# Performance work log

Measured on AMD Instinct MI355X. Metric: run time of the kernel, lower is better.

## Reference

```python
import jax, jax.numpy as jnp
import numpy as np

N = 100000      # nodes
E = 1600000     # edges
IN = 128        # in_channels
HID = 64        # hidden_channels
HEADS = 2       # gat_heads
NEG_SLOPE = 0.2 # PyG GATConv default leaky_relu slope


def setup_inputs() -> dict:
    key = jax.random.key(0)
    ks = jax.random.split(key, 8)
    x = jax.random.normal(ks[0], (N, IN), jnp.float32)
    edge_index = jax.random.randint(ks[1], (2, E), 0, N, jnp.int32)
    edge_weight = jax.random.uniform(ks[2], (E,), jnp.float32)
    gcn_w = jax.random.normal(ks[3], (IN, HID), jnp.float32) * (1.0 / np.sqrt(IN))
    gcn_b = jnp.zeros((HID,), jnp.float32)
    gat_w = jax.random.normal(ks[4], (HID, HEADS * HID), jnp.float32) * (1.0 / np.sqrt(HID))
    att_src = jax.random.normal(ks[5], (HEADS, HID), jnp.float32) * 0.1
    att_dst = jax.random.normal(ks[6], (HEADS, HID), jnp.float32) * 0.1
    gat_b = jnp.zeros((HID,), jnp.float32)
    return {"x": x, "edge_index": edge_index, "edge_weight": edge_weight,
            "gcn_w": gcn_w, "gcn_b": gcn_b, "gat_w": gat_w,
            "att_src": att_src, "att_dst": att_dst, "gat_b": gat_b}


def _gcn(x, w, b, src, dst, ew, n):
    # PyG GCNConv: add self-loops (weight 1), symmetric deg^{-1/2} norm.
    loop = jnp.arange(n, dtype=src.dtype)
    s = jnp.concatenate([src, loop])
    d = jnp.concatenate([dst, loop])
    wt = jnp.concatenate([ew, jnp.ones((n,), ew.dtype)])
    deg = jax.ops.segment_sum(wt, d, num_segments=n)              # in-degree (weighted)
    dinv = jnp.where(deg > 0, jax.lax.rsqrt(jnp.maximum(deg, 1e-12)), 0.0)
    norm = dinv[s] * wt * dinv[d]                                  # [E+N]
    h = x @ w                                                      # [N, HID]
    out = jax.ops.segment_sum(norm[:, None] * h[s], d, num_segments=n)
    return out + b


def _gat(x, w, a_src, a_dst, b, src, dst, n):
    # PyG GATConv: additive attention, self-loops, segment softmax over dst.
    h = (x @ w).reshape(n, HEADS, HID)                             # [N,H,C]
    score_s = jnp.einsum('nhc,hc->nh', h, a_src)                   # [N,H]
    score_d = jnp.einsum('nhc,hc->nh', h, a_dst)                   # [N,H]
    loop = jnp.arange(n, dtype=src.dtype)
    s = jnp.concatenate([src, loop])
    d = jnp.concatenate([dst, loop])
    alpha = score_s[s] + score_d[d]                                # [E+N,H]
    alpha = jnp.where(alpha >= 0, alpha, NEG_SLOPE * alpha)        # leaky_relu
    amax = jax.lax.stop_gradient(jax.ops.segment_max(alpha, d, num_segments=n))
    ex = jnp.exp(alpha - amax[d])
    denom = jax.ops.segment_sum(ex, d, num_segments=n)
    coef = ex / jnp.maximum(denom[d], 1e-16)                       # [E+N,H]
    out = jax.ops.segment_sum(coef[:, :, None] * h[s], d, num_segments=n)  # [N,H,C]
    return out.mean(axis=1) + b                                    # concat=False -> mean


def reference(x, edge_index, edge_weight, gcn_w, gcn_b, gat_w, att_src, att_dst, gat_b):
    src, dst = edge_index[0], edge_index[1]
    n = x.shape[0]
    h = jax.nn.relu(_gcn(x, gcn_w, gcn_b, src, dst, edge_weight, n))
    out = jax.nn.relu(_gat(h, gat_w, att_src, att_dst, gat_b, src, dst, n))
    return out
```

## Files before the change

kernel.cpp:

```cpp
#include <hip/hip_runtime.h>
#include <hip/hip_fp16.h>
#include <math.h>

#define N_NODES 100000
#define N_EDGES 1600000
#define IN_CH 128
#define HID 64
#define HEADS 2
#define NEG_SLOPE 0.2f

#define NB_SCAN ((N_NODES + 255) / 256)
#define SHARD_SZ 12500

static __device__ inline ushort f2h(float f) { return __half_as_ushort(__float2half(f)); }
static __device__ inline float h2f(ushort u) { return __half2float(__ushort_as_half(u)); }
static __device__ inline void h8f(uint4 u, float f[8]) {
    f[0] = h2f((ushort)(u.x & 0xffff)); f[1] = h2f((ushort)(u.x >> 16));
    f[2] = h2f((ushort)(u.y & 0xffff)); f[3] = h2f((ushort)(u.y >> 16));
    f[4] = h2f((ushort)(u.z & 0xffff)); f[5] = h2f((ushort)(u.z >> 16));
    f[6] = h2f((ushort)(u.w & 0xffff)); f[7] = h2f((ushort)(u.w >> 16));
}
static __device__ inline uint pack2(float a, float b) {
    return (uint)f2h(a) | ((uint)f2h(b) << 16);
}

__device__ inline float leaky(float a) { return (a >= 0.0f) ? a : NEG_SLOPE * a; }


__global__ void k_count(const int* __restrict__ dst, int* count) {
    int e = blockIdx.x * 256 + threadIdx.x;
    if (e < N_EDGES) atomicAdd(&count[dst[e]], 1);
}

__global__ void k_scan_a(const int* __restrict__ count, int* __restrict__ incl,
                         int* __restrict__ bsum) {
    __shared__ int sh[256];
    int tid = threadIdx.x;
    int g = blockIdx.x * 256 + tid;
    int v = (g < N_NODES) ? count[g] : 0;
    sh[tid] = v;
    __syncthreads();
    for (int off = 1; off < 256; off <<= 1) {
        int t = (tid >= off) ? sh[tid - off] : 0;
        __syncthreads();
        sh[tid] += t;
        __syncthreads();
    }
    if (g < N_NODES) incl[g] = sh[tid];
    if (tid == 255) bsum[blockIdx.x] = sh[255];
}

__global__ void k_scan_b(const int* __restrict__ bsum, int* __restrict__ boff) {
    __shared__ int sh[512];
    int tid = threadIdx.x;
    int v = (tid < NB_SCAN) ? bsum[tid] : 0;
    sh[tid] = v;
    __syncthreads();
    for (int off = 1; off < 512; off <<= 1) {
        int t = (tid >= off) ? sh[tid - off] : 0;
        __syncthreads();
        sh[tid] += t;
        __syncthreads();
    }
    if (tid < NB_SCAN) boff[tid] = sh[tid] - v;
}

__global__ void k_scan_c(const int* __restrict__ count, const int* __restrict__ incl,
                         const int* __restrict__ boff, int* rowptr, int* cursor) {
    int g = blockIdx.x * 256 + threadIdx.x;
    if (g >= N_NODES) return;
    int excl = incl[g] - count[g] + boff[blockIdx.x];
    rowptr[g] = excl;
    cursor[g] = excl;
    if (g == N_NODES - 1) rowptr[N_NODES] = incl[g] + boff[blockIdx.x];
}

__global__ void k_scatter(const int* __restrict__ src, const int* __restrict__ dst,
                          const float* __restrict__ ew,
                          int* cursor, int2* __restrict__ ep) {
    int shard = blockIdx.x & 7;
    int e = (blockIdx.x >> 3) * 256 + threadIdx.x;
    if (e >= N_EDGES) return;
    int d = dst[e];
    if (d / SHARD_SZ != shard) return;
    int pos = atomicAdd(&cursor[d], 1);
    ep[pos] = make_int2(src[e], __float_as_int(ew[e]));
}

__global__ void k_deg_dinv(const int* __restrict__ rowptr, const int2* __restrict__ ep,
                           float* __restrict__ dinv) {
    int n = blockIdx.x * 256 + threadIdx.x;
    if (n >= N_NODES) return;
    int r0 = rowptr[n], r1 = rowptr[n + 1];
    float deg = 1.0f;
    for (int i = r0; i < r1; ++i) deg += __int_as_float(ep[i].y);
    dinv[n] = rsqrtf(deg);
}


__global__ __launch_bounds__(256) void k_gemm1(const float* __restrict__ x,
                                               const float* __restrict__ w,
                                               ushort4* __restrict__ h1h) {
    __shared__ float sxT[64][65];
    __shared__ float sw[128][64];
    int t = threadIdx.x;
    int tx = t & 15, ty = t >> 4;
    int row0 = blockIdx.x * 64;
    for (int i = t; i < 128 * 16; i += 256)
        ((float4*)sw)[i] = ((const float4*)w)[i];
    float acc[4][4] = {};
    for (int c = 0; c < 2; ++c) {
        __syncthreads();
        for (int i = t; i < 64 * 16; i += 256) {
            int r = i >> 4, kq = i & 15;
            int row = row0 + r;
            float4 v = make_float4(0.f, 0.f, 0.f, 0.f);
            if (row < N_NODES) v = ((const float4*)x)[row * 32 + c * 16 + kq];
            int k = kq * 4;
            sxT[k][r] = v.x; sxT[k + 1][r] = v.y; sxT[k + 2][r] = v.z; sxT[k + 3][r] = v.w;
        }
        __syncthreads();
        #pragma unroll 8
        for (int k = 0; k < 64; ++k) {
            float a0 = sxT[k][ty * 4], a1 = sxT[k][ty * 4 + 1];
            float a2 = sxT[k][ty * 4 + 2], a3 = sxT[k][ty * 4 + 3];
            float4 bb = *(const float4*)&sw[c * 64 + k][tx * 4];
            acc[0][0] += a0 * bb.x; acc[0][1] += a0 * bb.y; acc[0][2] += a0 * bb.z; acc[0][3] += a0 * bb.w;
            acc[1][0] += a1 * bb.x; acc[1][1] += a1 * bb.y; acc[1][2] += a1 * bb.z; acc[1][3] += a1 * bb.w;
            acc[2][0] += a2 * bb.x; acc[2][1] += a2 * bb.y; acc[2][2] += a2 * bb.z; acc[2][3] += a2 * bb.w;
            acc[3][0] += a3 * bb.x; acc[3][1] += a3 * bb.y; acc[3][2] += a3 * bb.z; acc[3][3] += a3 * bb.w;
        }
    }
    #pragma unroll
    for (int i = 0; i < 4; ++i) {
        int row = row0 + ty * 4 + i;
        if (row < N_NODES) {
            ushort4 o;
            o.x = f2h(acc[i][0]); o.y = f2h(acc[i][1]); o.z = f2h(acc[i][2]); o.w = f2h(acc[i][3]);
            h1h[row * 16 + tx] = o;
        }
    }
}

__global__ __launch_bounds__(256) void k_gemm2(const uint4* __restrict__ a16,
                                               const float* __restrict__ w,
                                               const float* __restrict__ att_src,
                                               const float* __restrict__ att_dst,
                                               ushort4* __restrict__ h2h,
                                               float* __restrict__ ss, float* __restrict__ sd) {
    __shared__ float sxT[64][65];
    __shared__ float swh[64][64];
    int t = threadIdx.x;
    int tx = t & 15, ty = t >> 4;
    int tile = blockIdx.x >> 1, half = blockIdx.x & 1;
    int row0 = tile * 64;
    for (int i = t; i < 64 * 16; i += 256) {
        int k = i >> 4, cq = i & 15;
        float4 v = ((const float4*)(w + k * 128 + half * 64))[cq];
        ((float4*)&swh[k][cq * 4])[0] = v;
    }
    for (int i = t; i < 64 * 8; i += 256) {
        int r = i >> 3, j = i & 7;
        int row = row0 + r;
        float f[8] = {};
        if (row < N_NODES) { uint4 u = a16[row * 8 + j]; h8f(u, f); }
        int k = j * 8;
        #pragma unroll
        for (int m = 0; m < 8; ++m) sxT[k + m][r] = f[m];
    }
    __syncthreads();
    float acc[4][4] = {};
    #pragma unroll 8
    for (int k = 0; k < 64; ++k) {
        float a0 = sxT[k][ty * 4], a1 = sxT[k][ty * 4 + 1];
        float a2 = sxT[k][ty * 4 + 2], a3 = sxT[k][ty * 4 + 3];
        float4 bb = *(const float4*)&swh[k][tx * 4];
        acc[0][0] += a0 * bb.x; acc[0][1] += a0 * bb.y; acc[0][2] += a0 * bb.z; acc[0][3] += a0 * bb.w;
        acc[1][0] += a1 * bb.x; acc[1][1] += a1 * bb.y; acc[1][2] += a1 * bb.z; acc[1][3] += a1 * bb.w;
        acc[2][0] += a2 * bb.x; acc[2][1] += a2 * bb.y; acc[2][2] += a2 * bb.z; acc[2][3] += a2 * bb.w;
        acc[3][0] += a3 * bb.x; acc[3][1] += a3 * bb.y; acc[3][2] += a3 * bb.z; acc[3][3] += a3 * bb.w;
    }
    float as0 = att_src[half * 64 + tx * 4],     as1 = att_src[half * 64 + tx * 4 + 1];
    float as2 = att_src[half * 64 + tx * 4 + 2], as3 = att_src[half * 64 + tx * 4 + 3];
    float ad0 = att_dst[half * 64 + tx * 4],     ad1 = att_dst[half * 64 + tx * 4 + 1];
    float ad2 = att_dst[half * 64 + tx * 4 + 2], ad3 = att_dst[half * 64 + tx * 4 + 3];
    #pragma unroll
    for (int i = 0; i < 4; ++i) {
        int row = row0 + ty * 4 + i;
        float ps = acc[i][0] * as0 + acc[i][1] * as1 + acc[i][2] * as2 + acc[i][3] * as3;
        float pd = acc[i][0] * ad0 + acc[i][1] * ad1 + acc[i][2] * ad2 + acc[i][3] * ad3;
        #pragma unroll
        for (int off = 1; off < 16; off <<= 1) {
            ps += __shfl_xor(ps, off, 64);
            pd += __shfl_xor(pd, off, 64);
        }
        if (row < N_NODES) {
            if (tx == 0) { ss[row * 2 + half] = ps; sd[row * 2 + half] = pd; }
            ushort4 o;
            o.x = f2h(acc[i][0]); o.y = f2h(acc[i][1]); o.z = f2h(acc[i][2]); o.w = f2h(acc[i][3]);
            h2h[row * 32 + half * 16 + tx] = o;
        }
    }
}


__global__ void k_gcn_csr(const int* __restrict__ rowptr, const int2* __restrict__ ep,
                          const float* __restrict__ dinv,
                          const uint4* __restrict__ h1q, const float* __restrict__ b,
                          uint4* __restrict__ agg1h) {
    int t = threadIdx.x;
    int n = blockIdx.x * 4 + (t >> 6);
    if (n >= N_NODES) return;
    int lane = t & 63, q = lane >> 3, r = lane & 7;
    int r0 = rowptr[n], r1 = rowptr[n + 1];
    float dn = dinv[n];
    float acc[8] = {};
    if (q == 0) {
        float f[8]; h8f(h1q[n * 8 + r], f);
        #pragma unroll
        for (int j = 0; j < 8; ++j) acc[j] = dn * f[j];
    }
    for (int i = r0 + q; i < r1; i += 8) {
        int2 e = ep[i];
        float wl = dinv[e.x] * __int_as_float(e.y);
        float f[8]; h8f(h1q[e.x * 8 + r], f);
        #pragma unroll
        for (int j = 0; j < 8; ++j) acc[j] += wl * f[j];
    }
    #pragma unroll
    for (int off = 8; off < 64; off <<= 1) {
        #pragma unroll
        for (int j = 0; j < 8; ++j) acc[j] += __shfl_xor(acc[j], off, 64);
    }
    if (q == 0) {
        float4 b0 = ((const float4*)b)[2 * r], b1 = ((const float4*)b)[2 * r + 1];
        float v0 = fmaxf(acc[0] * dn + b0.x, 0.f), v1 = fmaxf(acc[1] * dn + b0.y, 0.f);
        float v2 = fmaxf(acc[2] * dn + b0.z, 0.f), v3 = fmaxf(acc[3] * dn + b0.w, 0.f);
        float v4 = fmaxf(acc[4] * dn + b1.x, 0.f), v5 = fmaxf(acc[5] * dn + b1.y, 0.f);
        float v6 = fmaxf(acc[6] * dn + b1.z, 0.f), v7 = fmaxf(acc[7] * dn + b1.w, 0.f);
        uint4 o;
        o.x = pack2(v0, v1); o.y = pack2(v2, v3); o.z = pack2(v4, v5); o.w = pack2(v6, v7);
        agg1h[n * 8 + r] = o;
    }
}

__global__ void k_gat_csr(const int* __restrict__ rowptr, const int2* __restrict__ ep,
                          const float* __restrict__ ss, const float* __restrict__ sd,
                          const uint4* __restrict__ h2q, const float* __restrict__ b,
                          float* __restrict__ out) {
    int t = threadIdx.x;
    int n = blockIdx.x * 4 + (t >> 6);
    if (n >= N_NODES) return;
    int lane = t & 63;
    int g = lane >> 4;
    int t16 = lane & 15;
    int head = t16 >> 3;
    int r = t16 & 7;
    int r0 = rowptr[n], r1 = rowptr[n + 1];
    float sdn = sd[n * 2 + head];
    float den = 0.f;
    float acc[8] = {};
    if (g == 0) {
        float exs = __expf(leaky(ss[n * 2 + head] + sdn));
        den = exs;
        float f[8]; h8f(h2q[n * 16 + t16], f);
        #pragma unroll
        for (int j = 0; j < 8; ++j) acc[j] = exs * f[j];
    }
    for (int i = r0 + g; i < r1; i += 4) {
        int s = ep[i].x;
        float ex = __expf(leaky(ss[s * 2 + head] + sdn));
        den += ex;
        float f[8]; h8f(h2q[s * 16 + t16], f);
        #pragma unroll
        for (int j = 0; j < 8; ++j) acc[j] += ex * f[j];
    }
    #pragma unroll
    for (int off = 16; off < 64; off <<= 1) {
        #pragma unroll
        for (int j = 0; j < 8; ++j) acc[j] += __shfl_xor(acc[j], off, 64);
        den += __shfl_xor(den, off, 64);
    }
    float inv = 1.0f / fmaxf(den, 1e-16f);
    #pragma unroll
    for (int j = 0; j < 8; ++j) acc[j] *= inv;
    float o[8];
    #pragma unroll
    for (int j = 0; j < 8; ++j) o[j] = 0.5f * (acc[j] + __shfl_xor(acc[j], 8, 64));
    if (g == 0 && head == 0) {
        float4 b0 = ((const float4*)b)[2 * r], b1 = ((const float4*)b)[2 * r + 1];
        float4* op = (float4*)(out + n * 64 + r * 8);
        op[0] = make_float4(fmaxf(o[0] + b0.x, 0.f), fmaxf(o[1] + b0.y, 0.f),
                            fmaxf(o[2] + b0.z, 0.f), fmaxf(o[3] + b0.w, 0.f));
        op[1] = make_float4(fmaxf(o[4] + b1.x, 0.f), fmaxf(o[5] + b1.y, 0.f),
                            fmaxf(o[6] + b1.z, 0.f), fmaxf(o[7] + b1.w, 0.f));
    }
}

extern "C" void kernel_launch(void* const* d_in, const int* in_sizes, int n_in,
                              void* d_out, int out_size, void* d_ws, size_t ws_size,
                              hipStream_t stream) {
    const float* x       = (const float*)d_in[0];
    const int*   eidx    = (const int*)d_in[1];
    const float* ew      = (const float*)d_in[2];
    const float* gcn_w   = (const float*)d_in[3];
    const float* gcn_b   = (const float*)d_in[4];
    const float* gat_w   = (const float*)d_in[5];
    const float* att_src = (const float*)d_in[6];
    const float* att_dst = (const float*)d_in[7];
    const float* gat_b   = (const float*)d_in[8];
    float* out = (float*)d_out;

    const int* src = eidx;
    const int* dst = eidx + N_EDGES;

    char* p = (char*)d_ws;
    ushort* agg1h = (ushort*)p; p += sizeof(ushort) * (size_t)N_NODES * 64;
    ushort* h1h   = (ushort*)p; p += sizeof(ushort) * (size_t)N_NODES * 64;
    ushort* h2h   = (ushort*)p; p += sizeof(ushort) * (size_t)N_NODES * 128;
    int2*  ep     = (int2*)p;   p += sizeof(int2) * (size_t)N_EDGES;
    int*   count  = (int*)p;    p += sizeof(int) * N_NODES;
    float* dinv   = (float*)p;  p += sizeof(float) * N_NODES;
    int*   incl   = (int*)p;    p += sizeof(int) * N_NODES;
    int*   rowptr = (int*)p;    p += sizeof(int) * (N_NODES + 1);
    int*   cursor = (int*)p;    p += sizeof(int) * N_NODES;
    float* ss     = (float*)p;  p += sizeof(float) * N_NODES * 2;
    float* sd     = (float*)p;  p += sizeof(float) * N_NODES * 2;
    int*   bsum   = (int*)p;    p += sizeof(int) * NB_SCAN;
    int*   boff   = (int*)p;    p += sizeof(int) * NB_SCAN;

    const int T = 256;
    const int NBe  = (N_EDGES + T - 1) / T;
    const int NBe8 = 8 * NBe;

    hipMemsetAsync(count, 0, sizeof(int) * N_NODES, stream);
    k_count<<<NBe, T, 0, stream>>>(dst, count);
    k_scan_a<<<NB_SCAN, T, 0, stream>>>(count, incl, bsum);
    k_scan_b<<<1, 512, 0, stream>>>(bsum, boff);
    k_scan_c<<<NB_SCAN, T, 0, stream>>>(count, incl, boff, rowptr, cursor);
    k_scatter<<<NBe8, T, 0, stream>>>(src, dst, ew, cursor, ep);
    k_deg_dinv<<<NB_SCAN, T, 0, stream>>>(rowptr, ep, dinv);

    k_gemm1<<<(N_NODES + 63) / 64, T, 0, stream>>>(x, gcn_w, (ushort4*)h1h);
    k_gcn_csr<<<(N_NODES + 3) / 4, T, 0, stream>>>(rowptr, ep, dinv, (const uint4*)h1h, gcn_b, (uint4*)agg1h);

    k_gemm2<<<((N_NODES + 63) / 64) * 2, T, 0, stream>>>((const uint4*)agg1h, gat_w, att_src, att_dst, (ushort4*)h2h, ss, sd);
    k_gat_csr<<<(N_NODES + 3) / 4, T, 0, stream>>>(rowptr, ep, ss, sd, (const uint4*)h2h, gat_b, out);
}
```

Measured before the change: 444.1 us.

## Record per-edge rank during counting to build CSR without scatter atomics

The counting pass now saves each edge's atomic return value as a rank and accumulates weighted degree with a float atomic. The scatter pass then computes positions directly from rowptr plus rank, with no cursor atomics and no 8-way sharded grid that re-read every edge eight times. The separate degree kernel is removed, and dinv is computed in the scan finalisation. The cost is an extra rank array write and read plus a float atomic per edge, and the order of float degree accumulation becomes nondeterministic.

```diff
diff --git a/kernel.cpp b/kernel.cpp
--- a/kernel.cpp
+++ b/kernel.cpp
@@ -10,7 +10,6 @@
 #define NEG_SLOPE 0.2f
 
 #define NB_SCAN ((N_NODES + 255) / 256)
-#define SHARD_SZ 12500
 
 static __device__ inline ushort f2h(float f) { return __half_as_ushort(__float2half(f)); }
 static __device__ inline float h2f(ushort u) { return __half2float(__ushort_as_half(u)); }
@@ -27,9 +26,13 @@
 __device__ inline float leaky(float a) { return (a >= 0.0f) ? a : NEG_SLOPE * a; }
 
 
-__global__ void k_count(const int* __restrict__ dst, int* count) {
+__global__ void k_count(const int* __restrict__ dst, const float* __restrict__ ew,
+                        int* count, float* degf, ushort* __restrict__ rank) {
     int e = blockIdx.x * 256 + threadIdx.x;
-    if (e < N_EDGES) atomicAdd(&count[dst[e]], 1);
+    if (e >= N_EDGES) return;
+    int d = dst[e];
+    rank[e] = (ushort)atomicAdd(&count[d], 1);
+    atomicAdd(&degf[d], ew[e]);
 }
 
 __global__ void k_scan_a(const int* __restrict__ count, int* __restrict__ incl,
@@ -66,35 +69,24 @@
 }
 
 __global__ void k_scan_c(const int* __restrict__ count, const int* __restrict__ incl,
-                         const int* __restrict__ boff, int* rowptr, int* cursor) {
+                         const int* __restrict__ boff, const float* __restrict__ degf,
+                         int* rowptr, float* __restrict__ dinv) {
     int g = blockIdx.x * 256 + threadIdx.x;
     if (g >= N_NODES) return;
     int excl = incl[g] - count[g] + boff[blockIdx.x];
     rowptr[g] = excl;
-    cursor[g] = excl;
+    dinv[g] = rsqrtf(1.0f + degf[g]);
     if (g == N_NODES - 1) rowptr[N_NODES] = incl[g] + boff[blockIdx.x];
 }
 
 __global__ void k_scatter(const int* __restrict__ src, const int* __restrict__ dst,
-                          const float* __restrict__ ew,
-                          int* cursor, int2* __restrict__ ep) {
-    int shard = blockIdx.x & 7;
-    int e = (blockIdx.x >> 3) * 256 + threadIdx.x;
+                          const float* __restrict__ ew, const ushort* __restrict__ rank,
+                          const int* __restrict__ rowptr, int2* __restrict__ ep) {
+    int e = blockIdx.x * 256 + threadIdx.x;
     if (e >= N_EDGES) return;
     int d = dst[e];
-    if (d / SHARD_SZ != shard) return;
-    int pos = atomicAdd(&cursor[d], 1);
+    int pos = rowptr[d] + (int)rank[e];
     ep[pos] = make_int2(src[e], __float_as_int(ew[e]));
-}
-
-__global__ void k_deg_dinv(const int* __restrict__ rowptr, const int2* __restrict__ ep,
-                           float* __restrict__ dinv) {
-    int n = blockIdx.x * 256 + threadIdx.x;
-    if (n >= N_NODES) return;
-    int r0 = rowptr[n], r1 = rowptr[n + 1];
-    float deg = 1.0f;
-    for (int i = r0; i < r1; ++i) deg += __int_as_float(ep[i].y);
-    dinv[n] = rsqrtf(deg);
 }
 
 
@@ -320,26 +312,25 @@
     ushort* h2h   = (ushort*)p; p += sizeof(ushort) * (size_t)N_NODES * 128;
     int2*  ep     = (int2*)p;   p += sizeof(int2) * (size_t)N_EDGES;
     int*   count  = (int*)p;    p += sizeof(int) * N_NODES;
+    float* degf   = (float*)p;  p += sizeof(float) * N_NODES;
     float* dinv   = (float*)p;  p += sizeof(float) * N_NODES;
     int*   incl   = (int*)p;    p += sizeof(int) * N_NODES;
     int*   rowptr = (int*)p;    p += sizeof(int) * (N_NODES + 1);
-    int*   cursor = (int*)p;    p += sizeof(int) * N_NODES;
     float* ss     = (float*)p;  p += sizeof(float) * N_NODES * 2;
     float* sd     = (float*)p;  p += sizeof(float) * N_NODES * 2;
     int*   bsum   = (int*)p;    p += sizeof(int) * NB_SCAN;
     int*   boff   = (int*)p;    p += sizeof(int) * NB_SCAN;
+    ushort* rank  = (ushort*)p; p += sizeof(ushort) * (size_t)N_EDGES;
 
     const int T = 256;
-    const int NBe  = (N_EDGES + T - 1) / T;
-    const int NBe8 = 8 * NBe;
-
-    hipMemsetAsync(count, 0, sizeof(int) * N_NODES, stream);
-    k_count<<<NBe, T, 0, stream>>>(dst, count);
+    const int NBe = (N_EDGES + T - 1) / T;
+
+    hipMemsetAsync(count, 0, sizeof(int) * N_NODES + sizeof(float) * N_NODES, stream);
+    k_count<<<NBe, T, 0, stream>>>(dst, ew, count, degf, rank);
     k_scan_a<<<NB_SCAN, T, 0, stream>>>(count, incl, bsum);
     k_scan_b<<<1, 512, 0, stream>>>(bsum, boff);
-    k_scan_c<<<NB_SCAN, T, 0, stream>>>(count, incl, boff, rowptr, cursor);
-    k_scatter<<<NBe8, T, 0, stream>>>(src, dst, ew, cursor, ep);
-    k_deg_dinv<<<NB_SCAN, T, 0, stream>>>(rowptr, ep, dinv);
+    k_scan_c<<<NB_SCAN, T, 0, stream>>>(count, incl, boff, degf, rowptr, dinv);
+    k_scatter<<<NBe, T, 0, stream>>>(src, dst, ew, rank, rowptr, ep);
 
     k_gemm1<<<(N_NODES + 63) / 64, T, 0, stream>>>(x, gcn_w, (ushort4*)h1h);
     k_gcn_csr<<<(N_NODES + 3) / 4, T, 0, stream>>>(rowptr, ep, dinv, (const uint4*)h1h, gcn_b, (uint4*)agg1h);
```

New measurement: 487.1 us. +9.7%, slower.

## Replace atomic CSR build with chunked LDS histogram and deterministic rank scatter

Applied to the files above, without the earlier changes.

Builds the CSR with a chunked counting sort instead of global atomics. Each block histograms one edge chunk for one node shard in shared memory and records each edge's 8-bit rank and per-chunk counts. A per-node prefix over chunks plus the global scan then gives every edge a deterministic slot, so the scatter needs no atomic cursor and no memset. This adds extra byte-table traffic (NCHUNK x N bytes) and assumes per-chunk, per-node counts fit in 8 bits.

```diff
diff --git a/kernel.cpp b/kernel.cpp
--- a/kernel.cpp
+++ b/kernel.cpp
@@ -10,7 +10,10 @@
 #define NEG_SLOPE 0.2f
 
 #define NB_SCAN ((N_NODES + 255) / 256)
-#define SHARD_SZ 12500
+#define SHARD 12500
+#define CHUNK_E 32768
+#define NCHUNK ((N_EDGES + CHUNK_E - 1) / CHUNK_E)
+#define BLK_PER_CHUNK (CHUNK_E / 256)
 
 static __device__ inline ushort f2h(float f) { return __half_as_ushort(__float2half(f)); }
 static __device__ inline float h2f(ushort u) { return __half2float(__ushort_as_half(u)); }
@@ -26,18 +29,46 @@
 
 __device__ inline float leaky(float a) { return (a >= 0.0f) ? a : NEG_SLOPE * a; }
 
-
-__global__ void k_count(const int* __restrict__ dst, int* count) {
-    int e = blockIdx.x * 256 + threadIdx.x;
-    if (e < N_EDGES) atomicAdd(&count[dst[e]], 1);
-}
-
-__global__ void k_scan_a(const int* __restrict__ count, int* __restrict__ incl,
-                         int* __restrict__ bsum) {
+__global__ __launch_bounds__(256) void k_hist(const int* __restrict__ dst,
+                                              unsigned char* __restrict__ rank8,
+                                              unsigned char* __restrict__ ctab8) {
+    __shared__ uint bins[SHARD];
+    int c = blockIdx.x >> 3, s = blockIdx.x & 7;
+    int base = s * SHARD;
+    for (int i = threadIdx.x; i < SHARD; i += 256) bins[i] = 0;
+    __syncthreads();
+    int e0 = c * CHUNK_E;
+    int e1 = e0 + CHUNK_E; if (e1 > N_EDGES) e1 = N_EDGES;
+    for (int e = e0 + threadIdx.x; e < e1; e += 256) {
+        int local = dst[e] - base;
+        if ((unsigned)local < SHARD) {
+            uint old = atomicAdd(&bins[local], 1u);
+            rank8[e] = (unsigned char)old;
+        }
+    }
+    __syncthreads();
+    unsigned char* cc = ctab8 + (size_t)c * N_NODES + base;
+    for (int i = threadIdx.x; i < SHARD; i += 256) cc[i] = (unsigned char)bins[i];
+}
+
+__global__ void k_scan_a(unsigned char* __restrict__ ctab8,
+                         int* __restrict__ cntN,
+                         int* __restrict__ incl, int* __restrict__ bsum) {
     __shared__ int sh[256];
     int tid = threadIdx.x;
     int g = blockIdx.x * 256 + tid;
-    int v = (g < N_NODES) ? count[g] : 0;
+    int v = 0;
+    if (g < N_NODES) {
+        int run = 0;
+        size_t idx = (size_t)g;
+        for (int c = 0; c < NCHUNK; ++c, idx += N_NODES) {
+            int cnt = ctab8[idx];
+            ctab8[idx] = (unsigned char)run;
+            run += cnt;
+        }
+        v = run;
+        cntN[g] = run;
+    }
     sh[tid] = v;
     __syncthreads();
     for (int off = 1; off < 256; off <<= 1) {
@@ -65,25 +96,30 @@
     if (tid < NB_SCAN) boff[tid] = sh[tid] - v;
 }
 
-__global__ void k_scan_c(const int* __restrict__ count, const int* __restrict__ incl,
-                         const int* __restrict__ boff, int* rowptr, int* cursor) {
+__global__ void k_scan_c(const int* __restrict__ cntN, const int* __restrict__ incl,
+                         const int* __restrict__ boff, int* rowptr) {
     int g = blockIdx.x * 256 + threadIdx.x;
     if (g >= N_NODES) return;
-    int excl = incl[g] - count[g] + boff[blockIdx.x];
+    int excl = incl[g] - cntN[g] + boff[blockIdx.x];
     rowptr[g] = excl;
-    cursor[g] = excl;
     if (g == N_NODES - 1) rowptr[N_NODES] = incl[g] + boff[blockIdx.x];
 }
 
 __global__ void k_scatter(const int* __restrict__ src, const int* __restrict__ dst,
                           const float* __restrict__ ew,
-                          int* cursor, int2* __restrict__ ep) {
-    int shard = blockIdx.x & 7;
-    int e = (blockIdx.x >> 3) * 256 + threadIdx.x;
+                          const unsigned char* __restrict__ rank8,
+                          const unsigned char* __restrict__ ctab8,
+                          const int* __restrict__ rowptr, int2* __restrict__ ep) {
+    int b = blockIdx.x;
+    int x = b & 7;
+    int g = b >> 3;
+    int j = g & (BLK_PER_CHUNK - 1);
+    int c = (g >> 7) * 8 + x;
+    if (c >= NCHUNK) return;
+    int e = c * CHUNK_E + j * 256 + threadIdx.x;
     if (e >= N_EDGES) return;
     int d = dst[e];
-    if (d / SHARD_SZ != shard) return;
-    int pos = atomicAdd(&cursor[d], 1);
+    int pos = rowptr[d] + (int)ctab8[(size_t)c * N_NODES + d] + (int)rank8[e];
     ep[pos] = make_int2(src[e], __float_as_int(ew[e]));
 }
 
@@ -319,26 +355,24 @@
     ushort* h1h   = (ushort*)p; p += sizeof(ushort) * (size_t)N_NODES * 64;
     ushort* h2h   = (ushort*)p; p += sizeof(ushort) * (size_t)N_NODES * 128;
     int2*  ep     = (int2*)p;   p += sizeof(int2) * (size_t)N_EDGES;
-    int*   count  = (int*)p;    p += sizeof(int) * N_NODES;
     float* dinv   = (float*)p;  p += sizeof(float) * N_NODES;
     int*   incl   = (int*)p;    p += sizeof(int) * N_NODES;
+    int*   cntN   = (int*)p;    p += sizeof(int) * N_NODES;
     int*   rowptr = (int*)p;    p += sizeof(int) * (N_NODES + 1);
-    int*   cursor = (int*)p;    p += sizeof(int) * N_NODES;
     float* ss     = (float*)p;  p += sizeof(float) * N_NODES * 2;
     float* sd     = (float*)p;  p += sizeof(float) * N_NODES * 2;
     int*   bsum   = (int*)p;    p += sizeof(int) * NB_SCAN;
     int*   boff   = (int*)p;    p += sizeof(int) * NB_SCAN;
+    unsigned char* ctab8 = (unsigned char*)p; p += (size_t)NCHUNK * N_NODES;
+    unsigned char* rank8 = (unsigned char*)p; p += (size_t)N_EDGES;
 
     const int T = 256;
-    const int NBe  = (N_EDGES + T - 1) / T;
-    const int NBe8 = 8 * NBe;
-
-    hipMemsetAsync(count, 0, sizeof(int) * N_NODES, stream);
-    k_count<<<NBe, T, 0, stream>>>(dst, count);
-    k_scan_a<<<NB_SCAN, T, 0, stream>>>(count, incl, bsum);
+
+    k_hist<<<NCHUNK * 8, T, 0, stream>>>(dst, rank8, ctab8);
+    k_scan_a<<<NB_SCAN, T, 0, stream>>>(ctab8, cntN, incl, bsum);
     k_scan_b<<<1, 512, 0, stream>>>(bsum, boff);
-    k_scan_c<<<NB_SCAN, T, 0, stream>>>(count, incl, boff, rowptr, cursor);
-    k_scatter<<<NBe8, T, 0, stream>>>(src, dst, ew, cursor, ep);
+    k_scan_c<<<NB_SCAN, T, 0, stream>>>(cntN, incl, boff, rowptr);
+    k_scatter<<<((NCHUNK + 7) / 8) * BLK_PER_CHUNK * 8, T, 0, stream>>>(src, dst, ew, rank8, ctab8, rowptr, ep);
     k_deg_dinv<<<NB_SCAN, T, 0, stream>>>(rowptr, ep, dinv);
 
     k_gemm1<<<(N_NODES + 63) / 64, T, 0, stream>>>(x, gcn_w, (ushort4*)h1h);
```

Result: faster. 404.5 us (-8.9%).
